# Kernel optimization log

Hardware: AMD Instinct MI355X
Metric: run time of the kernel (lower is better)

The kernel has to match this reference:

```python
import jax, jax.numpy as jnp
import numpy as np

NUM_HEADS = 16


def setup_inputs() -> dict:
    key = jax.random.key(0)
    k1, k2, k3 = jax.random.split(key, 3)
    b, s, d_model = 4, 4096, 1024
    x = jax.random.normal(k1, (b, s, d_model), dtype=jnp.float32)
    w_qkv = jax.random.normal(k2, (3 * d_model, d_model), dtype=jnp.float32) * 0.02
    b_qkv = jnp.zeros((3 * d_model,), dtype=jnp.float32)
    w_out = jax.random.normal(k3, (d_model, d_model), dtype=jnp.float32) * 0.02
    b_out = jnp.zeros((d_model,), dtype=jnp.float32)
    return {"x": x, "w_qkv": w_qkv, "b_qkv": b_qkv, "w_out": w_out, "b_out": b_out}


def reference(x, w_qkv, b_qkv, w_out, b_out):
    b, s, d_model = x.shape
    h = NUM_HEADS
    hd = d_model // h
    # qkv projection: [b, s, 3*d_model]
    qkv = jnp.einsum('bsd,ed->bse', x, w_qkv) + b_qkv
    # rearrange 'b s (three h d) -> three b h s d'
    qkv = qkv.reshape(b, s, 3, h, hd).transpose(2, 0, 3, 1, 4)  # [3, b, h, s, hd]
    q, k, v = qkv[0], qkv[1], qkv[2]
    # elu feature map
    q = jax.nn.elu(q) + 1.0
    k = jax.nn.elu(k) + 1.0
    # kv state: [b, h, hd, hd]
    kv = jnp.einsum('bhsd,bhse->bhde', k, v)
    # output: [b, h, s, hd]
    out = jnp.einsum('bhsd,bhde->bhse', q, kv)
    # normalization (elementwise divide by per-feature k sum, broadcast over s)
    k_sum = k.sum(axis=-2, keepdims=True)  # [b, h, 1, hd]
    out = out / (k_sum + 1e-6)
    # 'b h s d -> b s (h d)'
    out = out.transpose(0, 2, 1, 3).reshape(b, s, d_model)
    return jnp.einsum('bsd,ed->bse', out, w_out) + b_out
```

## Files before the change

### kernel.cpp

```cpp
#include <hip/hip_runtime.h>
#include <stdint.h>

typedef float f32x4 __attribute__((ext_vector_type(4)));
typedef __bf16 bf16x8 __attribute__((ext_vector_type(8)));
typedef unsigned short u16;
typedef u16 u16x8 __attribute__((ext_vector_type(8)));

__device__ __forceinline__ u16 f2bf(float f) {
  uint32_t u = __builtin_bit_cast(uint32_t, f);
  return (u16)((u + 0x7fffu + ((u >> 16) & 1u)) >> 16);
}
__device__ __forceinline__ float bf2f(u16 h) {
  uint32_t u = ((uint32_t)h) << 16;
  return __builtin_bit_cast(float, u);
}
__device__ __forceinline__ float elup1(float x) {
  return x > 0.f ? x + 1.f : __expf(x);
}
__device__ __forceinline__ void gll16(const void* g, void* l) {
  __builtin_amdgcn_global_load_lds(
      (const __attribute__((address_space(1))) unsigned int*)g,
      (__attribute__((address_space(3))) unsigned int*)l, 16, 0, 0);
}

#define BAR() __builtin_amdgcn_s_barrier()
#define VMC(n) asm volatile("s_waitcnt vmcnt(" #n ")" ::: "memory")

__global__ void cvt_all_kernel(const float* __restrict__ x, u16* __restrict__ xb,
                               const float* __restrict__ wq, u16* __restrict__ wqb,
                               const float* __restrict__ wo, u16* __restrict__ wob) {
  int i = blockIdx.x * 256 + threadIdx.x;
  const float* in;
  u16* out;
  if (i < 4194304) {
    in = x; out = xb;
  } else if (i < 4980736) {
    in = wq; out = wqb; i -= 4194304;
  } else {
    in = wo; out = wob; i -= 4980736;
  }
  float4 f = ((const float4*)in)[i];
  ushort4 o;
  o.x = f2bf(f.x); o.y = f2bf(f.y); o.z = f2bf(f.z); o.w = f2bf(f.w);
  ((ushort4*)out)[i] = o;
}

template <int EPI>
__global__ __launch_bounds__(512, 2)
void gemm256(const u16* __restrict__ A, const u16* __restrict__ B,
             const float* __restrict__ bias, void* __restrict__ Cout,
             int N, int K, int nbj) {
  __shared__ __align__(16) u16 lds[65536];
  const int tid = threadIdx.x;
  const int wave = tid >> 6, lane = tid & 63;
  const int fr = lane & 15, fq = lane >> 4;
  const int wm = wave >> 2, wn = wave & 3;

  const int nwg = gridDim.x;
  const int cpx = nwg >> 3;
  const int swz = (blockIdx.x & 7) * cpx + (blockIdx.x >> 3);
  const int bi = swz / nbj, bj = swz % nbj;

  const u16* Ab = A + (size_t)bi * 256 * K;
  const u16* Bb = B + (size_t)bj * 256 * K;

  const int l8 = lane >> 3;
  const int cswz = ((lane & 7) ^ l8) << 3;
  const int r6 = wave * 8 + l8;

#define STAGE_A(d, h, k0)                                                      \
  { _Pragma("unroll")                                                          \
    for (int i_ = 0; i_ < 2; ++i_) {                                           \
      int gr_ = i_ * 128 + (h) * 64 + r6;                                      \
      gll16(Ab + (size_t)gr_ * K + (k0) + cswz,                                \
            &lds[((d) * 32768 + (h) * 16384 + i_ * 8192 + wave * 1024) >> 1]); \
    } }

#define STAGE_B(d, h, k0)                                                      \
  { _Pragma("unroll")                                                          \
    for (int i_ = 0; i_ < 2; ++i_) {                                           \
      int r_ = i_ * 64 + r6;                                                   \
      int gr_ = (r_ >> 5) * 64 + (h) * 32 + (r_ & 31);                         \
      gll16(Bb + (size_t)gr_ * K + (k0) + cswz,                                \
            &lds[(65536 + (d) * 32768 + (h) * 16384 + i_ * 8192 + wave * 1024) >> 1]); \
    } }

  const int xorc = (fr & 7) << 4;
  const int acol[2] = {(fq * 16) ^ xorc, (64 + fq * 16) ^ xorc};
  const int arow = (wm * 64 + fr) * 128;
  const int brow = (wn * 32 + fr) * 128;

#define LDSV(off) (*(const bf16x8*)&lds[(off) >> 1])

  f32x4 acc[8][4] = {};
  bf16x8 af[4][2];
  bf16x8 bfr[2][2][2];

#define READ_A(d, mh)                                                          \
  { _Pragma("unroll")                                                          \
    for (int ks = 0; ks < 2; ++ks) {                                           \
      _Pragma("unroll")                                                        \
      for (int mm = 0; mm < 4; ++mm)                                           \
        af[mm][ks] = LDSV((d) * 32768 + (mh) * 16384 + arow + mm * 2048 + acol[ks]); \
    } }

#define READ_B(d, nh)                                                          \
  { _Pragma("unroll")                                                          \
    for (int ks = 0; ks < 2; ++ks) {                                           \
      _Pragma("unroll")                                                        \
      for (int nn = 0; nn < 2; ++nn)                                           \
        bfr[nh][nn][ks] = LDSV(65536 + (d) * 32768 + (nh) * 16384 + brow + nn * 2048 + acol[ks]); \
    } }

#define MFMA_Q(mh, nh)                                                         \
  { __builtin_amdgcn_s_setprio(1);                                             \
    _Pragma("unroll")                                                          \
    for (int ks = 0; ks < 2; ++ks) {                                           \
      _Pragma("unroll")                                                        \
      for (int mm = 0; mm < 4; ++mm) {                                         \
        _Pragma("unroll")                                                      \
        for (int nn = 0; nn < 2; ++nn)                                         \
          acc[(mh) * 4 + mm][(nh) * 2 + nn] = __builtin_amdgcn_mfma_f32_16x16x32_bf16( \
              af[mm][ks], bfr[nh][nn][ks], acc[(mh) * 4 + mm][(nh) * 2 + nn], 0, 0, 0); \
      } }                                                                      \
    __builtin_amdgcn_s_setprio(0); }

  const int NT = K >> 6;
  STAGE_A(0, 0, 0); STAGE_B(0, 0, 0); STAGE_B(0, 1, 0); STAGE_A(0, 1, 0);
  STAGE_A(1, 0, 64); STAGE_B(1, 0, 64); STAGE_B(1, 1, 64);
  VMC(6);
  BAR();

  for (int t = 0; t < NT; ++t) {
    const int d = t & 1;
    const int k1 = (t + 1) << 6, k2 = (t + 2) << 6;
    if (t + 1 < NT) STAGE_A(d ^ 1, 1, k1);
    READ_B(d, 0); READ_A(d, 0);
    MFMA_Q(0, 0);
    READ_B(d, 1);
    MFMA_Q(0, 1);
    BAR();
    if (t + 2 < NT) { STAGE_A(d, 0, k2); STAGE_B(d, 0, k2); }
    READ_A(d, 1);
    MFMA_Q(1, 1);
    if (t + 2 < NT) STAGE_B(d, 1, k2);
    MFMA_Q(1, 0);
    if (t < NT - 2) { VMC(6); } else { VMC(0); }
    BAR();
  }

  const int wrow = wm * 128, wcol = wn * 64;
  if (EPI == 0) {
    const bool do_elu = (bj * 256) < 2048;
    float bv[4];
#pragma unroll
    for (int n = 0; n < 4; ++n) bv[n] = bias[bj * 256 + wcol + n * 16 + fr];
    u16* wbuf = &lds[wave * 8192];
    const int lrow = lane >> 3, lcol = (lane & 7) * 8;
#pragma unroll
    for (int ch = 0; ch < 2; ++ch) {
#pragma unroll
      for (int m2 = 0; m2 < 4; ++m2)
#pragma unroll
        for (int n = 0; n < 4; ++n)
#pragma unroll
          for (int r = 0; r < 4; ++r) {
            float v = acc[ch * 4 + m2][n][r] + bv[n];
            if (do_elu) v = elup1(v);
            wbuf[(m2 * 16 + fq * 4 + r) * 72 + n * 16 + fr] = f2bf(v);
          }
#pragma unroll
      for (int i = 0; i < 8; ++i) {
        bf16x8 val = *(const bf16x8*)&wbuf[(i * 8 + lrow) * 72 + lcol];
        const int rowg = bi * 256 + wrow + ch * 64 + i * 8 + lrow;
        *(bf16x8*)&((u16*)Cout)[(size_t)rowg * N + bj * 256 + wcol + lcol] = val;
      }
    }
  } else {
#pragma unroll
    for (int n = 0; n < 4; ++n) {
      const int colg = bj * 256 + wcol + n * 16 + fr;
      const float bv = bias[colg];
#pragma unroll
      for (int m = 0; m < 8; ++m)
#pragma unroll
        for (int r = 0; r < 4; ++r) {
          const int rowg = bi * 256 + wrow + m * 16 + fq * 4 + r;
          ((float*)Cout)[(size_t)rowg * N + colg] = acc[m][n][r] + bv;
        }
    }
  }
#undef STAGE_A
#undef STAGE_B
#undef READ_A
#undef READ_B
#undef MFMA_Q
#undef LDSV
}

__global__ __launch_bounds__(256)
void kv_state_kernel(const u16* __restrict__ qkv, float* __restrict__ pkv,
                     float* __restrict__ pks) {
  const int bh = blockIdx.x, chunk = blockIdx.y;
  const int b = bh >> 4, h = bh & 15;
  const int t = threadIdx.x;
  __shared__ float sK[16][68];
  __shared__ float sV[16][68];
  const int dg = (t & 15) * 4;
  const int eg = (t >> 4) * 4;
  f32x4 acc0 = {}, acc1 = {}, acc2 = {}, acc3 = {};
  f32x4 ak4 = {};
  const size_t rowbase = ((size_t)b * 4096 + (size_t)chunk * 512) * 3072;
  const u16* kp = qkv + rowbase + 1024 + h * 64;
  const u16* vp = qkv + rowbase + 2048 + h * 64;
  const int lhalf = t >> 7, lr = (t >> 3) & 15, lc = (t & 7) * 8;
  const u16* lsrc = lhalf ? vp : kp;
  float* ldst = lhalf ? &sV[lr][lc] : &sK[lr][lc];
  for (int s0 = 0; s0 < 512; s0 += 16) {
    u16x8 v8 = *(const u16x8*)&lsrc[(size_t)(s0 + lr) * 3072 + lc];
#pragma unroll
    for (int j = 0; j < 8; ++j) ldst[j] = bf2f(v8[j]);
    __syncthreads();
#pragma unroll 4
    for (int sl = 0; sl < 16; ++sl) {
      const f32x4 kv4 = *(const f32x4*)&sK[sl][dg];
      const f32x4 vv4 = *(const f32x4*)&sV[sl][eg];
      acc0 += kv4[0] * vv4;
      acc1 += kv4[1] * vv4;
      acc2 += kv4[2] * vv4;
      acc3 += kv4[3] * vv4;
      ak4 += kv4;
    }
    __syncthreads();
  }
  float* outp = pkv + ((size_t)chunk * 64 + bh) * 4096;
  *(f32x4*)&outp[(dg + 0) * 64 + eg] = acc0;
  *(f32x4*)&outp[(dg + 1) * 64 + eg] = acc1;
  *(f32x4*)&outp[(dg + 2) * 64 + eg] = acc2;
  *(f32x4*)&outp[(dg + 3) * 64 + eg] = acc3;
  if (t < 16) *(f32x4*)&pks[((size_t)chunk * 64 + bh) * 64 + dg] = ak4;
}

__global__ __launch_bounds__(256)
void kv_reduce_kernel(const float* __restrict__ pkv, const float* __restrict__ pks,
                      float* __restrict__ kvn) {
  const int bh = blockIdx.x;
  const int t = threadIdx.x;
  __shared__ float sks[64];
  if (t < 64) {
    float s = 0.f;
    for (int c = 0; c < 8; ++c) s += pks[((size_t)c * 64 + bh) * 64 + t];
    sks[t] = s + 1e-6f;
  }
  __syncthreads();
#pragma unroll
  for (int j = 0; j < 16; ++j) {
    int idx = t + j * 256;
    float s = 0.f;
    for (int c = 0; c < 8; ++c) s += pkv[((size_t)c * 64 + bh) * 4096 + idx];
    kvn[(size_t)bh * 4096 + idx] = s / sks[idx & 63];
  }
}

__global__ __launch_bounds__(256)
void attn_out_kernel(const u16* __restrict__ qkv, const float* __restrict__ kvn,
                     u16* __restrict__ attn) {
  const int bh = blockIdx.x;
  const int b = bh >> 4, h = bh & 15;
  const int stile = blockIdx.y;
  const int wave = threadIdx.x >> 6, lane = threadIdx.x & 63;
  const int s0 = stile * 64 + wave * 16;
  const int fr = lane & 15, fq = lane >> 4;
  __shared__ u16 sO[4][16 * 72];
  const float* kv = kvn + (size_t)bh * 4096;
  bf16x8 bfrag[2][4];
#pragma unroll
  for (int ks = 0; ks < 2; ++ks)
#pragma unroll
    for (int n = 0; n < 4; ++n) {
      u16x8 tmp;
#pragma unroll
      for (int j = 0; j < 8; ++j)
        tmp[j] = f2bf(kv[(size_t)(ks * 32 + fq * 8 + j) * 64 + n * 16 + fr]);
      bfrag[ks][n] = __builtin_bit_cast(bf16x8, tmp);
    }
  const u16* q = qkv + (size_t)b * 4096 * 3072 + h * 64;
  f32x4 acc[4] = {};
#pragma unroll
  for (int ks = 0; ks < 2; ++ks) {
    bf16x8 af = *(const bf16x8*)&q[(size_t)(s0 + fr) * 3072 + ks * 32 + fq * 8];
#pragma unroll
    for (int n = 0; n < 4; ++n)
      acc[n] = __builtin_amdgcn_mfma_f32_16x16x32_bf16(af, bfrag[ks][n], acc[n], 0, 0, 0);
  }
  u16* wb = &sO[wave][0];
#pragma unroll
  for (int n = 0; n < 4; ++n)
#pragma unroll
    for (int r = 0; r < 4; ++r)
      wb[(fq * 4 + r) * 72 + n * 16 + fr] = f2bf(acc[n][r]);
  u16* ap = attn + (size_t)b * 4096 * 1024 + h * 64;
  const int lrow = lane >> 3, lcol = (lane & 7) * 8;
#pragma unroll
  for (int i = 0; i < 2; ++i) {
    bf16x8 val = *(const bf16x8*)&wb[(i * 8 + lrow) * 72 + lcol];
    *(bf16x8*)&ap[(size_t)(s0 + i * 8 + lrow) * 1024 + lcol] = val;
  }
}

extern "C" void kernel_launch(void* const* d_in, const int* in_sizes, int n_in,
                              void* d_out, int out_size, void* d_ws, size_t ws_size,
                              hipStream_t stream) {
  const float* x     = (const float*)d_in[0];
  const float* w_qkv = (const float*)d_in[1];
  const float* b_qkv = (const float*)d_in[2];
  const float* w_out = (const float*)d_in[3];
  const float* b_out = (const float*)d_in[4];
  float* out = (float*)d_out;

  const int M = 16384, Dm = 1024, N3 = 3072;

  char* ws = (char*)d_ws;
  u16* xb     = (u16*)(ws);
  u16* wqb    = (u16*)(ws + 33554432);
  u16* wob    = (u16*)(ws + 39845888);
  u16* qkvb   = (u16*)(ws + 41943040);
  u16* attnb  = (u16*)(ws + 142606336);
  float* pkv  = (float*)(ws + 176160768);
  float* pks  = (float*)(ws + 184549376);
  float* kvn  = (float*)(ws + 184680448);

  cvt_all_kernel<<<20480, 256, 0, stream>>>(x, xb, w_qkv, wqb, w_out, wob);

  gemm256<0><<<(M / 256) * (N3 / 256), 512, 0, stream>>>(xb, wqb, b_qkv, qkvb, N3, Dm, N3 / 256);
  kv_state_kernel<<<dim3(64, 8), 256, 0, stream>>>(qkvb, pkv, pks);
  kv_reduce_kernel<<<64, 256, 0, stream>>>(pkv, pks, kvn);
  attn_out_kernel<<<dim3(64, 64), 256, 0, stream>>>(qkvb, kvn, attnb);
  gemm256<1><<<(M / 256) * (Dm / 256), 512, 0, stream>>>(attnb, wob, b_out, out, Dm, Dm, Dm / 256);
}
```

Measured before the change: 241.7 us.

## Shrink GEMM tiles to 128x128 and restructure kv_state thread mapping

```diff
diff --git a/kernel.cpp b/kernel.cpp
--- a/kernel.cpp
+++ b/kernel.cpp
@@ -24,6 +24,8 @@
 }
 
 #define BAR() __builtin_amdgcn_s_barrier()
+#define LGKM0() asm volatile("s_waitcnt lgkmcnt(0)" ::: "memory")
+#define SCHED0() __builtin_amdgcn_sched_barrier(0)
 #define VMC(n) asm volatile("s_waitcnt vmcnt(" #n ")" ::: "memory")
 
 __global__ void cvt_all_kernel(const float* __restrict__ x, u16* __restrict__ xb,
@@ -46,155 +48,132 @@
 }
 
 template <int EPI>
-__global__ __launch_bounds__(512, 2)
-void gemm256(const u16* __restrict__ A, const u16* __restrict__ B,
+__global__ __launch_bounds__(256, 2)
+void gemm128(const u16* __restrict__ A, const u16* __restrict__ B,
              const float* __restrict__ bias, void* __restrict__ Cout,
              int N, int K, int nbj) {
-  __shared__ __align__(16) u16 lds[65536];
+  __shared__ __align__(16) u16 lds[32768];
   const int tid = threadIdx.x;
   const int wave = tid >> 6, lane = tid & 63;
   const int fr = lane & 15, fq = lane >> 4;
-  const int wm = wave >> 2, wn = wave & 3;
+  const int wm = wave >> 1, wn = wave & 1;
 
   const int nwg = gridDim.x;
   const int cpx = nwg >> 3;
   const int swz = (blockIdx.x & 7) * cpx + (blockIdx.x >> 3);
   const int bi = swz / nbj, bj = swz % nbj;
 
-  const u16* Ab = A + (size_t)bi * 256 * K;
-  const u16* Bb = B + (size_t)bj * 256 * K;
-
-  const int l8 = lane >> 3;
-  const int cswz = ((lane & 7) ^ l8) << 3;
-  const int r6 = wave * 8 + l8;
-
-#define STAGE_A(d, h, k0)                                                      \
+  const u16* Ab = A + (size_t)bi * 128 * K;
+  const u16* Bb = B + (size_t)bj * 128 * K;
+
+  const int cswz = ((tid & 7) ^ ((tid >> 3) & 7)) << 3;
+  const int srow = tid >> 3;
+
+#define STAGE_ALL(d, k0)                                                       \
   { _Pragma("unroll")                                                          \
-    for (int i_ = 0; i_ < 2; ++i_) {                                           \
-      int gr_ = i_ * 128 + (h) * 64 + r6;                                      \
-      gll16(Ab + (size_t)gr_ * K + (k0) + cswz,                                \
-            &lds[((d) * 32768 + (h) * 16384 + i_ * 8192 + wave * 1024) >> 1]); \
-    } }
-
-#define STAGE_B(d, h, k0)                                                      \
-  { _Pragma("unroll")                                                          \
-    for (int i_ = 0; i_ < 2; ++i_) {                                           \
-      int r_ = i_ * 64 + r6;                                                   \
-      int gr_ = (r_ >> 5) * 64 + (h) * 32 + (r_ & 31);                         \
-      gll16(Bb + (size_t)gr_ * K + (k0) + cswz,                                \
-            &lds[(65536 + (d) * 32768 + (h) * 16384 + i_ * 8192 + wave * 1024) >> 1]); \
-    } }
+    for (int i_ = 0; i_ < 4; ++i_)                                             \
+      gll16(Ab + (size_t)(i_ * 32 + srow) * K + (k0) + cswz,                   \
+            &lds[((d) * 32768 + i_ * 4096 + wave * 1024) >> 1]);               \
+    _Pragma("unroll")                                                          \
+    for (int i_ = 0; i_ < 4; ++i_)                                             \
+      gll16(Bb + (size_t)(i_ * 32 + srow) * K + (k0) + cswz,                   \
+            &lds[((d) * 32768 + 16384 + i_ * 4096 + wave * 1024) >> 1]);       \
+  }
 
   const int xorc = (fr & 7) << 4;
   const int acol[2] = {(fq * 16) ^ xorc, (64 + fq * 16) ^ xorc};
   const int arow = (wm * 64 + fr) * 128;
-  const int brow = (wn * 32 + fr) * 128;
+  const int brow = (wn * 64 + fr) * 128;
 
 #define LDSV(off) (*(const bf16x8*)&lds[(off) >> 1])
 
-  f32x4 acc[8][4] = {};
-  bf16x8 af[4][2];
-  bf16x8 bfr[2][2][2];
-
-#define READ_A(d, mh)                                                          \
+  f32x4 acc[4][4] = {};
+  bf16x8 af[4][2], bf[4][2];
+
+#define READ_ALL(d)                                                            \
   { _Pragma("unroll")                                                          \
     for (int ks = 0; ks < 2; ++ks) {                                           \
       _Pragma("unroll")                                                        \
+      for (int nn = 0; nn < 4; ++nn)                                           \
+        bf[nn][ks] = LDSV((d) * 32768 + 16384 + brow + nn * 2048 + acol[ks]);  \
+      _Pragma("unroll")                                                        \
       for (int mm = 0; mm < 4; ++mm)                                           \
-        af[mm][ks] = LDSV((d) * 32768 + (mh) * 16384 + arow + mm * 2048 + acol[ks]); \
+        af[mm][ks] = LDSV((d) * 32768 + arow + mm * 2048 + acol[ks]);          \
     } }
 
-#define READ_B(d, nh)                                                          \
-  { _Pragma("unroll")                                                          \
-    for (int ks = 0; ks < 2; ++ks) {                                           \
-      _Pragma("unroll")                                                        \
-      for (int nn = 0; nn < 2; ++nn)                                           \
-        bfr[nh][nn][ks] = LDSV(65536 + (d) * 32768 + (nh) * 16384 + brow + nn * 2048 + acol[ks]); \
-    } }
-
-#define MFMA_Q(mh, nh)                                                         \
+#define MFMA_ALL()                                                             \
   { __builtin_amdgcn_s_setprio(1);                                             \
     _Pragma("unroll")                                                          \
     for (int ks = 0; ks < 2; ++ks) {                                           \
       _Pragma("unroll")                                                        \
       for (int mm = 0; mm < 4; ++mm) {                                         \
         _Pragma("unroll")                                                      \
-        for (int nn = 0; nn < 2; ++nn)                                         \
-          acc[(mh) * 4 + mm][(nh) * 2 + nn] = __builtin_amdgcn_mfma_f32_16x16x32_bf16( \
-              af[mm][ks], bfr[nh][nn][ks], acc[(mh) * 4 + mm][(nh) * 2 + nn], 0, 0, 0); \
+        for (int nn = 0; nn < 4; ++nn)                                         \
+          acc[mm][nn] = __builtin_amdgcn_mfma_f32_16x16x32_bf16(               \
+              af[mm][ks], bf[nn][ks], acc[mm][nn], 0, 0, 0);                   \
       } }                                                                      \
     __builtin_amdgcn_s_setprio(0); }
 
   const int NT = K >> 6;
-  STAGE_A(0, 0, 0); STAGE_B(0, 0, 0); STAGE_B(0, 1, 0); STAGE_A(0, 1, 0);
-  STAGE_A(1, 0, 64); STAGE_B(1, 0, 64); STAGE_B(1, 1, 64);
-  VMC(6);
+  STAGE_ALL(0, 0);
+  STAGE_ALL(1, 64);
+  VMC(8);
   BAR();
 
   for (int t = 0; t < NT; ++t) {
     const int d = t & 1;
-    const int k1 = (t + 1) << 6, k2 = (t + 2) << 6;
-    if (t + 1 < NT) STAGE_A(d ^ 1, 1, k1);
-    READ_B(d, 0); READ_A(d, 0);
-    MFMA_Q(0, 0);
-    READ_B(d, 1);
-    MFMA_Q(0, 1);
+    READ_ALL(d);
+    LGKM0(); SCHED0();
     BAR();
-    if (t + 2 < NT) { STAGE_A(d, 0, k2); STAGE_B(d, 0, k2); }
-    READ_A(d, 1);
-    MFMA_Q(1, 1);
-    if (t + 2 < NT) STAGE_B(d, 1, k2);
-    MFMA_Q(1, 0);
-    if (t < NT - 2) { VMC(6); } else { VMC(0); }
+    if (t + 2 < NT) STAGE_ALL(d, (t + 2) << 6);
+    MFMA_ALL();
+    if (t + 2 < NT) { VMC(8); }
+    else if (t + 1 < NT) { VMC(0); }
     BAR();
   }
 
-  const int wrow = wm * 128, wcol = wn * 64;
+  const int wrow = wm * 64, wcol = wn * 64;
   if (EPI == 0) {
-    const bool do_elu = (bj * 256) < 2048;
+    const bool do_elu = (bj * 128) < 2048;
     float bv[4];
 #pragma unroll
-    for (int n = 0; n < 4; ++n) bv[n] = bias[bj * 256 + wcol + n * 16 + fr];
-    u16* wbuf = &lds[wave * 8192];
+    for (int n = 0; n < 4; ++n) bv[n] = bias[bj * 128 + wcol + n * 16 + fr];
+    u16* wbuf = &lds[wave * 2048];
     const int lrow = lane >> 3, lcol = (lane & 7) * 8;
 #pragma unroll
-    for (int ch = 0; ch < 2; ++ch) {
-#pragma unroll
-      for (int m2 = 0; m2 < 4; ++m2)
-#pragma unroll
-        for (int n = 0; n < 4; ++n)
-#pragma unroll
-          for (int r = 0; r < 4; ++r) {
-            float v = acc[ch * 4 + m2][n][r] + bv[n];
-            if (do_elu) v = elup1(v);
-            wbuf[(m2 * 16 + fq * 4 + r) * 72 + n * 16 + fr] = f2bf(v);
-          }
-#pragma unroll
-      for (int i = 0; i < 8; ++i) {
+    for (int mm = 0; mm < 4; ++mm) {
+#pragma unroll
+      for (int n = 0; n < 4; ++n)
+#pragma unroll
+        for (int r = 0; r < 4; ++r) {
+          float v = acc[mm][n][r] + bv[n];
+          if (do_elu) v = elup1(v);
+          wbuf[(fq * 4 + r) * 72 + n * 16 + fr] = f2bf(v);
+        }
+#pragma unroll
+      for (int i = 0; i < 2; ++i) {
         bf16x8 val = *(const bf16x8*)&wbuf[(i * 8 + lrow) * 72 + lcol];
-        const int rowg = bi * 256 + wrow + ch * 64 + i * 8 + lrow;
-        *(bf16x8*)&((u16*)Cout)[(size_t)rowg * N + bj * 256 + wcol + lcol] = val;
+        const int rowg = bi * 128 + wrow + mm * 16 + i * 8 + lrow;
+        *(bf16x8*)&((u16*)Cout)[(size_t)rowg * N + bj * 128 + wcol + lcol] = val;
       }
     }
   } else {
 #pragma unroll
     for (int n = 0; n < 4; ++n) {
-      const int colg = bj * 256 + wcol + n * 16 + fr;
+      const int colg = bj * 128 + wcol + n * 16 + fr;
       const float bv = bias[colg];
 #pragma unroll
-      for (int m = 0; m < 8; ++m)
+      for (int mm = 0; mm < 4; ++mm)
 #pragma unroll
         for (int r = 0; r < 4; ++r) {
-          const int rowg = bi * 256 + wrow + m * 16 + fq * 4 + r;
-          ((float*)Cout)[(size_t)rowg * N + colg] = acc[m][n][r] + bv;
+          const int rowg = bi * 128 + wrow + mm * 16 + fq * 4 + r;
+          ((float*)Cout)[(size_t)rowg * N + colg] = acc[mm][n][r] + bv;
         }
     }
   }
-#undef STAGE_A
-#undef STAGE_B
-#undef READ_A
-#undef READ_B
-#undef MFMA_Q
+#undef STAGE_ALL
+#undef READ_ALL
+#undef MFMA_ALL
 #undef LDSV
 }
 
@@ -204,12 +183,15 @@
   const int bh = blockIdx.x, chunk = blockIdx.y;
   const int b = bh >> 4, h = bh & 15;
   const int t = threadIdx.x;
-  __shared__ float sK[16][68];
-  __shared__ float sV[16][68];
-  const int dg = (t & 15) * 4;
-  const int eg = (t >> 4) * 4;
-  f32x4 acc0 = {}, acc1 = {}, acc2 = {}, acc3 = {};
-  f32x4 ak4 = {};
+  __shared__ float smem[16416];
+  float (*sK)[68] = (float(*)[68])smem;
+  float (*sV)[68] = (float(*)[68])(smem + 1088);
+  const int s4 = t >> 6;
+  const int dq = (t >> 3) & 7;
+  const int eq = t & 7;
+  const int d8 = dq * 8, e8 = eq * 8;
+  f32x4 accA[8] = {}, accB[8] = {};
+  float ak[8] = {};
   const size_t rowbase = ((size_t)b * 4096 + (size_t)chunk * 512) * 3072;
   const u16* kp = qkv + rowbase + 1024 + h * 64;
   const u16* vp = qkv + rowbase + 2048 + h * 64;
@@ -221,24 +203,56 @@
 #pragma unroll
     for (int j = 0; j < 8; ++j) ldst[j] = bf2f(v8[j]);
     __syncthreads();
-#pragma unroll 4
-    for (int sl = 0; sl < 16; ++sl) {
-      const f32x4 kv4 = *(const f32x4*)&sK[sl][dg];
-      const f32x4 vv4 = *(const f32x4*)&sV[sl][eg];
-      acc0 += kv4[0] * vv4;
-      acc1 += kv4[1] * vv4;
-      acc2 += kv4[2] * vv4;
-      acc3 += kv4[3] * vv4;
-      ak4 += kv4;
+#pragma unroll
+    for (int j = 0; j < 4; ++j) {
+      const int sl = j * 4 + s4;
+      f32x4 ka = *(const f32x4*)&sK[sl][d8];
+      f32x4 kb = *(const f32x4*)&sK[sl][d8 + 4];
+      f32x4 va = *(const f32x4*)&sV[sl][e8];
+      f32x4 vb = *(const f32x4*)&sV[sl][e8 + 4];
+#pragma unroll
+      for (int di = 0; di < 4; ++di) {
+        accA[di] += ka[di] * va;
+        accB[di] += ka[di] * vb;
+        accA[4 + di] += kb[di] * va;
+        accB[4 + di] += kb[di] * vb;
+      }
+      if (eq == 0) {
+#pragma unroll
+        for (int di = 0; di < 4; ++di) {
+          ak[di] += ka[di];
+          ak[4 + di] += kb[di];
+        }
+      }
     }
     __syncthreads();
   }
+  float* red = smem;
+  float* redk = smem + 16384;
   float* outp = pkv + ((size_t)chunk * 64 + bh) * 4096;
-  *(f32x4*)&outp[(dg + 0) * 64 + eg] = acc0;
-  *(f32x4*)&outp[(dg + 1) * 64 + eg] = acc1;
-  *(f32x4*)&outp[(dg + 2) * 64 + eg] = acc2;
-  *(f32x4*)&outp[(dg + 3) * 64 + eg] = acc3;
-  if (t < 16) *(f32x4*)&pks[((size_t)chunk * 64 + bh) * 64 + dg] = ak4;
+  float* outk = pks + ((size_t)chunk * 64 + bh) * 64;
+  for (int di = 0; di < 8; ++di) {
+    __syncthreads();
+    *(f32x4*)&red[t * 8] = accA[di];
+    *(f32x4*)&red[t * 8 + 4] = accB[di];
+    if (eq == 0) redk[s4 * 8 + dq] = ak[di];
+    __syncthreads();
+    if (t < 64) {
+      const int rdq = t >> 3, req = t & 7;
+      f32x4 sA = {}, sB = {};
+#pragma unroll
+      for (int s = 0; s < 4; ++s) {
+        const int src = (s * 64 + rdq * 8 + req) * 8;
+        sA += *(const f32x4*)&red[src];
+        sB += *(const f32x4*)&red[src + 4];
+      }
+      float* op = outp + (rdq * 8 + di) * 64 + req * 8;
+      *(f32x4*)op = sA;
+      *(f32x4*)(op + 4) = sB;
+      if (req == 0)
+        outk[rdq * 8 + di] = redk[rdq] + redk[8 + rdq] + redk[16 + rdq] + redk[24 + rdq];
+    }
+  }
 }
 
 __global__ __launch_bounds__(256)
@@ -332,9 +346,9 @@
 
   cvt_all_kernel<<<20480, 256, 0, stream>>>(x, xb, w_qkv, wqb, w_out, wob);
 
-  gemm256<0><<<(M / 256) * (N3 / 256), 512, 0, stream>>>(xb, wqb, b_qkv, qkvb, N3, Dm, N3 / 256);
+  gemm128<0><<<(M / 128) * (N3 / 128), 256, 0, stream>>>(xb, wqb, b_qkv, qkvb, N3, Dm, N3 / 128);
   kv_state_kernel<<<dim3(64, 8), 256, 0, stream>>>(qkvb, pkv, pks);
   kv_reduce_kernel<<<64, 256, 0, stream>>>(pkv, pks, kvn);
   attn_out_kernel<<<dim3(64, 64), 256, 0, stream>>>(qkvb, kvn, attnb);
-  gemm256<1><<<(M / 256) * (Dm / 256), 512, 0, stream>>>(attnb, wob, b_out, out, Dm, Dm, Dm / 256);
-}
+  gemm128<1><<<(M / 128) * (Dm / 128), 256, 0, stream>>>(attnb, wob, b_out, out, Dm, Dm, Dm / 128);
+}
```

Measured after the change: 254.2 us. 5.2% more time.
